# Optimization experiments

Measured on AMD Instinct MI355X. Metric: run time of the kernel, lower is better.

## Reference

```python
import jax, jax.numpy as jnp
import numpy as np

N_NODES = 50000
N_EDGES = 600000
EMB_DIM = 128
HIDDEN = 128
BN_EPS = 1e-5


def setup_inputs() -> dict:
    key = jax.random.key(0)
    ks = jax.random.split(key, 8)
    s_in = 1.0 / np.sqrt(EMB_DIM)
    s_h = 1.0 / np.sqrt(HIDDEN)
    return {
        "x_idx": jnp.arange(N_NODES, dtype=jnp.int32),
        "edge_index": jax.random.randint(ks[0], (2, N_EDGES), 0, N_NODES, dtype=jnp.int32),
        "emb_table": jax.random.normal(ks[1], (N_NODES, EMB_DIM), jnp.float32),
        # ClusterGCNConv: lin_out (bias=False) and lin_root (bias=False)
        "W_out": jax.random.uniform(ks[2], (HIDDEN, EMB_DIM), jnp.float32, -s_in, s_in),
        "W_root": jax.random.uniform(ks[3], (HIDDEN, EMB_DIM), jnp.float32, -s_in, s_in),
        "bn0_gamma": jnp.ones((HIDDEN,), jnp.float32),
        "bn0_beta": jnp.zeros((HIDDEN,), jnp.float32),
        # SGConv 1 (K=1, add_self_loops=True, Linear with bias)
        "W_sg1": jax.random.uniform(ks[4], (HIDDEN, HIDDEN), jnp.float32, -s_h, s_h),
        "b_sg1": jnp.zeros((HIDDEN,), jnp.float32),
        "bn1_gamma": jnp.ones((HIDDEN,), jnp.float32),
        "bn1_beta": jnp.zeros((HIDDEN,), jnp.float32),
        # SGConv 2 (final layer)
        "W_sg2": jax.random.uniform(ks[5], (HIDDEN, HIDDEN), jnp.float32, -s_h, s_h),
        "b_sg2": jnp.zeros((HIDDEN,), jnp.float32),
    }


def _cluster_gcn(x, row, col, W_out, W_root, n):
    # PyG ClusterGCNConv (add_self_loops=False, diag_lambda=0, bias=False):
    # out[c] = sum_{(r->c)} (1/deg(c)) * x[r];  return out @ W_out^T + x @ W_root^T
    deg = jax.ops.segment_sum(jnp.ones_like(col, dtype=x.dtype), col, num_segments=n)
    deg_inv = 1.0 / jnp.maximum(deg, 1.0)
    msg = x[row] * deg_inv[col][:, None]                  # [E, D]
    agg = jax.ops.segment_sum(msg, col, num_segments=n)   # [N, D]
    return agg @ W_out.T + x @ W_root.T


def _sg_conv(x, row, col, W, b, n):
    # PyG SGConv K=1 with gcn_norm: A_hat = D^{-1/2}(A+I)D^{-1/2}, then Linear.
    loop = jnp.arange(n, dtype=row.dtype)
    r = jnp.concatenate([row, loop])
    c = jnp.concatenate([col, loop])
    deg = jax.ops.segment_sum(jnp.ones_like(c, dtype=x.dtype), c, num_segments=n)
    dis = jnp.where(deg > 0, jax.lax.rsqrt(jnp.maximum(deg, 1e-12)), 0.0)
    ew = dis[r] * dis[c]                                   # [E+N]
    agg = jax.ops.segment_sum(x[r] * ew[:, None], c, num_segments=n)
    return agg @ W.T + b


def _bn(x, gamma, beta):
    # BatchNorm1d in training mode: batch statistics, biased variance.
    mu = x.mean(axis=0)
    var = ((x - mu) ** 2).mean(axis=0)
    return (x - mu) * jax.lax.rsqrt(var + BN_EPS) * gamma + beta


def reference(x_idx, edge_index, emb_table, W_out, W_root, bn0_gamma, bn0_beta,
              W_sg1, b_sg1, bn1_gamma, bn1_beta, W_sg2, b_sg2):
    n = emb_table.shape[0]
    row, col = edge_index[0], edge_index[1]
    x = emb_table[x_idx]                                   # [N, D]
    # layer 0: ClusterGCNConv -> BN -> ReLU (dropout p=0)
    x = _cluster_gcn(x, row, col, W_out, W_root, n)
    x = jax.nn.relu(_bn(x, bn0_gamma, bn0_beta))
    # layer 1: SGConv -> BN -> ReLU
    x = _sg_conv(x, row, col, W_sg1, b_sg1, n)
    x = jax.nn.relu(_bn(x, bn1_gamma, bn1_beta))
    # final SGConv
    return _sg_conv(x, row, col, W_sg2, b_sg2, n)
```

## Files before the change

kernel.cpp:

```cpp
#include <hip/hip_runtime.h>
#include <stdint.h>

#define NN 50000
#define NE 600000
#define DD 128
#define BN_EPS 1e-5f

typedef __attribute__((ext_vector_type(8))) short short8;
typedef __attribute__((ext_vector_type(4))) float f32x4;

__device__ __forceinline__ float bf2f(uint16_t u) {
    union { uint32_t u; float f; } v; v.u = ((uint32_t)u) << 16; return v.f;
}
__device__ __forceinline__ uint16_t f2bf(float f) {
    union { float f; uint32_t u; } v; v.f = f;
    return (uint16_t)((v.u + 0x7FFFu + ((v.u >> 16) & 1u)) >> 16);
}
__device__ __forceinline__ float lo16(uint32_t v) { return bf2f((uint16_t)(v & 0xFFFFu)); }
__device__ __forceinline__ float hi16(uint32_t v) { return bf2f((uint16_t)(v >> 16)); }

__global__ void k_zero(uint4* __restrict__ p, int n16) {
    int i = blockIdx.x * 256 + threadIdx.x;
    if (i < n16) p[i] = make_uint4(0u, 0u, 0u, 0u);
}

#define EB ((NE + 255) / 256)
#define VB ((NN * 32) / 256)
#define WB 32
__global__ void k_pre(const int* __restrict__ ei, int* __restrict__ cnt,
                      const int* __restrict__ x_idx, const float* __restrict__ emb,
                      uint16_t* __restrict__ xb,
                      const float* __restrict__ Wa, const float* __restrict__ Wb_,
                      const float* __restrict__ Wc, const float* __restrict__ Wd,
                      uint16_t* __restrict__ wb) {
    int b = blockIdx.x;
    if (b < EB) {
        int e = b * 256 + threadIdx.x;
        if (e < NE) atomicAdd(&cnt[ei[NE + e]], 1);
    } else if (b < EB + VB) {
        int idx = (b - EB) * 256 + threadIdx.x;
        int node = idx >> 5, c4 = (idx & 31) << 2;
        int src = x_idx[node];
        float4 v = *(const float4*)(emb + (size_t)src * DD + c4);
        ushort4 o;
        o.x = f2bf(v.x); o.y = f2bf(v.y); o.z = f2bf(v.z); o.w = f2bf(v.w);
        *(ushort4*)(xb + (size_t)node * DD + c4) = o;
    } else {
        int idx = (b - EB - VB) * 256 + threadIdx.x;
        int w = idx >> 11, rem = idx & 2047;
        const float* src = (w == 0) ? Wa : (w == 1) ? Wb_ : (w == 2) ? Wc : Wd;
        float4 v0 = *(const float4*)(src + rem * 8);
        float4 v1 = *(const float4*)(src + rem * 8 + 4);
        uint4 pk;
        pk.x = (uint32_t)f2bf(v0.x) | ((uint32_t)f2bf(v0.y) << 16);
        pk.y = (uint32_t)f2bf(v0.z) | ((uint32_t)f2bf(v0.w) << 16);
        pk.z = (uint32_t)f2bf(v1.x) | ((uint32_t)f2bf(v1.y) << 16);
        pk.w = (uint32_t)f2bf(v1.z) | ((uint32_t)f2bf(v1.w) << 16);
        *(uint4*)(wb + (size_t)w * 16384 + rem * 8) = pk;
    }
}

__global__ void k_alloc(const int* __restrict__ cnt, int* __restrict__ cursor,
                        int* __restrict__ off, int* __restrict__ fillp,
                        float* __restrict__ deginv, float* __restrict__ dis) {
    int i = blockIdx.x * 256 + threadIdx.x;
    int lane = threadIdx.x & 63;
    int deg = (i < NN) ? cnt[i] : 0;
    int v = deg;
    #pragma unroll
    for (int d = 1; d < 64; d <<= 1) {
        int t = __shfl_up(v, d, 64);
        if (lane >= d) v += t;
    }
    int total = __shfl(v, 63, 64);
    int wbase = 0;
    if (lane == 63) wbase = atomicAdd(cursor, total);
    wbase = __shfl(wbase, 63, 64);
    int base = wbase + v - deg;
    if (i < NN) {
        off[i] = base;
        fillp[i] = base;
        deginv[i] = 1.0f / fmaxf((float)deg, 1.0f);
        dis[i] = rsqrtf((float)deg + 1.0f);
    }
}

__global__ void k_fill(const int* __restrict__ ei, int* __restrict__ fillp,
                       int* __restrict__ csr_row) {
    int e = blockIdx.x * 256 + threadIdx.x;
    if (e < NE) {
        int c = ei[NE + e];
        int p = atomicAdd(&fillp[c], 1);
        csr_row[p] = ei[e];
    }
}

template<int MODE>
__global__ __launch_bounds__(256)
void k_agg(const uint16_t* __restrict__ X, const int* __restrict__ off,
           const int* __restrict__ cnt, const int* __restrict__ csr_row,
           const float* __restrict__ deginv, const float* __restrict__ dis,
           uint16_t* __restrict__ aggb) {
    int gw = blockIdx.x * 4 + (threadIdx.x >> 6);
    int lane = threadIdx.x & 63;
    int hl = lane & 31;
    int node = gw * 2 + (lane >> 5);
    if (node >= NN) return;
    float a0 = 0.0f, a1 = 0.0f, a2 = 0.0f, a3 = 0.0f;
    if (MODE == 1) {
        uint2 v = ((const uint2*)(X + (size_t)node * DD))[hl];
        a0 = lo16(v.x); a1 = hi16(v.x); a2 = lo16(v.y); a3 = hi16(v.y);
    }
    int s = off[node], deg = cnt[node];
    int degO = __shfl(deg, lane ^ 32, 64);
    int mdeg = max(deg, degO);
    for (int b = 0; b < mdeg; b += 32) {
        int c32 = min(deg - b, 32);
        int idxv = (hl < c32) ? csr_row[s + b + hl] : 0;
        int steps = min(mdeg - b, 32);
        int i = 0;
        for (; i + 8 <= steps; i += 8) {
            uint2 v[8]; float w[8];
            #pragma unroll
            for (int u = 0; u < 8; ++u) {
                int r = __shfl(idxv, (lane & 32) + i + u, 64);
                w[u] = (b + i + u < deg) ? 1.0f : 0.0f;
                v[u] = ((const uint2*)(X + (size_t)r * DD))[hl];
            }
            #pragma unroll
            for (int u = 0; u < 8; ++u) {
                a0 = fmaf(w[u], lo16(v[u].x), a0);
                a1 = fmaf(w[u], hi16(v[u].x), a1);
                a2 = fmaf(w[u], lo16(v[u].y), a2);
                a3 = fmaf(w[u], hi16(v[u].y), a3);
            }
        }
        if (i + 4 <= steps) {
            uint2 v[4]; float w[4];
            #pragma unroll
            for (int u = 0; u < 4; ++u) {
                int r = __shfl(idxv, (lane & 32) + i + u, 64);
                w[u] = (b + i + u < deg) ? 1.0f : 0.0f;
                v[u] = ((const uint2*)(X + (size_t)r * DD))[hl];
            }
            #pragma unroll
            for (int u = 0; u < 4; ++u) {
                a0 = fmaf(w[u], lo16(v[u].x), a0);
                a1 = fmaf(w[u], hi16(v[u].x), a1);
                a2 = fmaf(w[u], lo16(v[u].y), a2);
                a3 = fmaf(w[u], hi16(v[u].y), a3);
            }
            i += 4;
        }
        for (; i < steps; ++i) {
            int r = __shfl(idxv, (lane & 32) + i, 64);
            float w = (b + i < deg) ? 1.0f : 0.0f;
            uint2 v = ((const uint2*)(X + (size_t)r * DD))[hl];
            a0 = fmaf(w, lo16(v.x), a0);
            a1 = fmaf(w, hi16(v.x), a1);
            a2 = fmaf(w, lo16(v.y), a2);
            a3 = fmaf(w, hi16(v.y), a3);
        }
    }
    float sc = (MODE == 1) ? dis[node] : deginv[node];
    a0 *= sc; a1 *= sc; a2 *= sc; a3 *= sc;
    uint2 o;
    o.x = (uint32_t)f2bf(a0) | ((uint32_t)f2bf(a1) << 16);
    o.y = (uint32_t)f2bf(a2) | ((uint32_t)f2bf(a3) << 16);
    ((uint2*)(aggb + (size_t)node * DD))[hl] = o;
}

template<bool DUAL, bool STATS, bool BIAS, bool STORE_BF16>
__global__ __launch_bounds__(256, 2)
void k_gemm(const uint16_t* __restrict__ A1, const uint16_t* __restrict__ A2,
            const uint16_t* __restrict__ Wb1, const uint16_t* __restrict__ Wb2,
            const float* __restrict__ bias, float* __restrict__ Hf,
            uint16_t* __restrict__ Hb, float* __restrict__ stats) {
    constexpr int NW = DUAL ? 2 : 1;
    __shared__ uint16_t Wlds[NW * 128 * 128];
    const int t = threadIdx.x;
    const int lane = t & 63, wid = t >> 6;
    const int l15 = lane & 15, kgrp = lane >> 4;
    const int wm = (wid >> 1) * 64, wn = (wid & 1) * 64;
    const int m0 = blockIdx.x * 128;

    short8 a1r[4][4];
    #pragma unroll
    for (int m = 0; m < 4; ++m) {
        int row = min(m0 + wm + m * 16 + l15, NN - 1);
        const uint16_t* ap = A1 + (size_t)row * DD + kgrp * 8;
        #pragma unroll
        for (int ks = 0; ks < 4; ++ks)
            a1r[m][ks] = *(const short8*)(ap + ks * 32);
    }
    #pragma unroll
    for (int w = 0; w < NW; ++w) {
        const uint16_t* Ws = w ? Wb2 : Wb1;
        #pragma unroll
        for (int it = 0; it < 8; ++it) {
            int idx = it * 256 + t;
            int row = idx >> 4, c16 = idx & 15;
            uint4 v = *(const uint4*)(Ws + row * DD + c16 * 8);
            uint32_t boff = (uint32_t)(w * 32768 + row * 256 + ((c16 * 16) ^ ((row & 7) << 4)));
            *(uint4*)((char*)Wlds + boff) = v;
        }
    }
    __syncthreads();

    f32x4 acc[4][4];
    #pragma unroll
    for (int m = 0; m < 4; ++m)
        #pragma unroll
        for (int n = 0; n < 4; ++n) acc[m][n] = f32x4{0.0f, 0.0f, 0.0f, 0.0f};

    short8 a2r[4][4];
    if (DUAL) {
        #pragma unroll
        for (int m = 0; m < 4; ++m) {
            int row = min(m0 + wm + m * 16 + l15, NN - 1);
            const uint16_t* ap = A2 + (size_t)row * DD + kgrp * 8;
            #pragma unroll
            for (int ks = 0; ks < 4; ++ks)
                a2r[m][ks] = *(const short8*)(ap + ks * 32);
        }
    }
    #pragma unroll
    for (int ph = 0; ph < NW; ++ph) {
        #pragma unroll
        for (int ks = 0; ks < 4; ++ks) {
            short8 b[4];
            int kb = ks * 64 + (kgrp << 4);
            #pragma unroll
            for (int n = 0; n < 4; ++n) {
                int row = wn + n * 16 + l15;
                b[n] = *(const short8*)((const char*)Wlds + ph * 32768
                                        + row * 256 + (kb ^ ((row & 7) << 4)));
            }
            #pragma unroll
            for (int m = 0; m < 4; ++m)
                #pragma unroll
                for (int n = 0; n < 4; ++n)
                    acc[m][n] = __builtin_amdgcn_mfma_f32_16x16x32_bf16(
                        (ph ? a2r : a1r)[m][ks], b[n], acc[m][n], 0, 0, 0);
        }
    }
    float* stc = STATS ? stats + (wid & 3) * 256 : nullptr;
    #pragma unroll
    for (int n = 0; n < 4; ++n) {
        int col = wn + n * 16 + l15;
        float bb = BIAS ? bias[col] : 0.0f;
        float ssum = 0.0f, ssq = 0.0f;
        #pragma unroll
        for (int m = 0; m < 4; ++m) {
            int rbase = m0 + wm + m * 16 + kgrp * 4;
            #pragma unroll
            for (int i = 0; i < 4; ++i) {
                int gr = rbase + i;
                if (gr < NN) {
                    float v = acc[m][n][i] + bb;
                    if (STORE_BF16) Hb[(size_t)gr * DD + col] = f2bf(v);
                    else            Hf[(size_t)gr * DD + col] = v;
                    ssum += v; ssq += v * v;
                }
            }
        }
        if (STATS) {
            ssum += __shfl_xor(ssum, 16, 64);
            ssum += __shfl_xor(ssum, 32, 64);
            ssq  += __shfl_xor(ssq, 16, 64);
            ssq  += __shfl_xor(ssq, 32, 64);
            if (lane < 16) {
                atomicAdd(&stc[col], ssum);
                atomicAdd(&stc[128 + col], ssq);
            }
        }
    }
}

__global__ __launch_bounds__(256)
void k_bnrelu(const uint16_t* __restrict__ Hb, const float* __restrict__ st,
              const float* __restrict__ gamma, const float* __restrict__ beta,
              const float* __restrict__ dis, uint16_t* __restrict__ xb) {
    __shared__ float s_sc[128], s_of[128];
    int t = threadIdx.x;
    if (t < 128) {
        const float invn = 1.0f / (float)NN;
        float sum = st[t] + st[256 + t] + st[512 + t] + st[768 + t];
        float sq  = st[128 + t] + st[384 + t] + st[640 + t] + st[896 + t];
        float mean = sum * invn;
        float var = sq * invn - mean * mean;
        float sc = gamma[t] * rsqrtf(var + BN_EPS);
        s_sc[t] = sc;
        s_of[t] = beta[t] - mean * sc;
    }
    __syncthreads();
    int idx = blockIdx.x * 256 + t;
    int node = idx >> 4, c8 = (idx & 15) << 3;
    if (node >= NN) return;
    float d = dis[node];
    uint4 h = *(const uint4*)(Hb + (size_t)node * DD + c8);
    uint32_t hw[4] = {h.x, h.y, h.z, h.w};
    uint32_t ow[4];
    #pragma unroll
    for (int j = 0; j < 4; ++j) {
        int c = c8 + j * 2;
        float v0 = fmaxf(lo16(hw[j]) * s_sc[c]     + s_of[c],     0.0f) * d;
        float v1 = fmaxf(hi16(hw[j]) * s_sc[c + 1] + s_of[c + 1], 0.0f) * d;
        ow[j] = (uint32_t)f2bf(v0) | ((uint32_t)f2bf(v1) << 16);
    }
    uint4 o = make_uint4(ow[0], ow[1], ow[2], ow[3]);
    *(uint4*)(xb + (size_t)node * DD + c8) = o;
}

extern "C" void kernel_launch(void* const* d_in, const int* in_sizes, int n_in,
                              void* d_out, int out_size, void* d_ws, size_t ws_size,
                              hipStream_t stream) {
    const int* x_idx   = (const int*)d_in[0];
    const int* ei      = (const int*)d_in[1];
    const float* emb   = (const float*)d_in[2];
    const float* W_out = (const float*)d_in[3];
    const float* W_root= (const float*)d_in[4];
    const float* g0    = (const float*)d_in[5];
    const float* be0   = (const float*)d_in[6];
    const float* W1    = (const float*)d_in[7];
    const float* b1    = (const float*)d_in[8];
    const float* g1    = (const float*)d_in[9];
    const float* be1   = (const float*)d_in[10];
    const float* W2    = (const float*)d_in[11];
    const float* b2    = (const float*)d_in[12];
    float* out = (float*)d_out;

    char* ws = (char*)d_ws;
    size_t o = 0;
    auto carve = [&](size_t bytes) -> void* {
        void* p = ws + o;
        o = (o + bytes + 255) & ~(size_t)255;
        return p;
    };
    int* cnt      = (int*)carve((size_t)NN * 4);
    int* cursor   = (int*)carve(4);
    float* st0    = (float*)carve(1024 * 4);
    float* st1    = (float*)carve(1024 * 4);
    size_t zlen = o;
    int* fillp    = (int*)carve((size_t)NN * 4);
    int* off      = (int*)carve((size_t)NN * 4);
    float* deginv = (float*)carve((size_t)NN * 4);
    float* dis    = (float*)carve((size_t)NN * 4);
    int* csr_row  = (int*)carve((size_t)NE * 4);
    uint16_t* xb  = (uint16_t*)carve((size_t)NN * DD * 2);
    uint16_t* aggb= (uint16_t*)carve((size_t)NN * DD * 2);
    uint16_t* hb  = (uint16_t*)carve((size_t)NN * DD * 2);
    uint16_t* wb  = (uint16_t*)carve((size_t)4 * 16384 * 2);

    const int ZB = (int)((zlen / 16 + 255) / 256);
    const int NB = (NN + 255) / 256;
    const int GB = (NN + 127) / 128;
    const int AB = (NN / 2 + 3) / 4;
    const int BB = (NN * 16 + 255) / 256;

    k_zero<<<ZB, 256, 0, stream>>>((uint4*)ws, (int)(zlen / 16));
    k_pre<<<EB + VB + WB, 256, 0, stream>>>(ei, cnt, x_idx, emb, xb,
                                            W_out, W_root, W1, W2, wb);
    k_alloc<<<NB, 256, 0, stream>>>(cnt, cursor, off, fillp, deginv, dis);
    k_fill<<<EB, 256, 0, stream>>>(ei, fillp, csr_row);

    k_agg<0><<<AB, 256, 0, stream>>>(xb, off, cnt, csr_row, deginv, dis, aggb);
    k_gemm<true, true, false, true><<<GB, 256, 0, stream>>>(
        aggb, xb, wb, wb + 16384, nullptr, nullptr, hb, st0);
    k_bnrelu<<<BB, 256, 0, stream>>>(hb, st0, g0, be0, dis, xb);

    k_agg<1><<<AB, 256, 0, stream>>>(xb, off, cnt, csr_row, deginv, dis, aggb);
    k_gemm<false, true, true, true><<<GB, 256, 0, stream>>>(
        aggb, nullptr, wb + 32768, nullptr, b1, nullptr, hb, st1);
    k_bnrelu<<<BB, 256, 0, stream>>>(hb, st1, g1, be1, dis, xb);

    k_agg<1><<<AB, 256, 0, stream>>>(xb, off, cnt, csr_row, deginv, dis, aggb);
    k_gemm<false, false, true, false><<<GB, 256, 0, stream>>>(
        aggb, nullptr, wb + 49152, nullptr, b2, out, nullptr, nullptr);
}
```

Measured before the change: 229.2 us.

## Shrink GEMM block tile to 64 rows with 16-row per-wave strips

```diff
diff --git a/kernel.cpp b/kernel.cpp
--- a/kernel.cpp
+++ b/kernel.cpp
@@ -171,7 +171,7 @@
 }
 
 template<bool DUAL, bool STATS, bool BIAS, bool STORE_BF16>
-__global__ __launch_bounds__(256, 2)
+__global__ __launch_bounds__(256, DUAL ? 2 : 4)
 void k_gemm(const uint16_t* __restrict__ A1, const uint16_t* __restrict__ A2,
             const uint16_t* __restrict__ Wb1, const uint16_t* __restrict__ Wb2,
             const float* __restrict__ bias, float* __restrict__ Hf,
@@ -181,17 +181,15 @@
     const int t = threadIdx.x;
     const int lane = t & 63, wid = t >> 6;
     const int l15 = lane & 15, kgrp = lane >> 4;
-    const int wm = (wid >> 1) * 64, wn = (wid & 1) * 64;
-    const int m0 = blockIdx.x * 128;
-
-    short8 a1r[4][4];
-    #pragma unroll
-    for (int m = 0; m < 4; ++m) {
-        int row = min(m0 + wm + m * 16 + l15, NN - 1);
+    const int r0 = blockIdx.x * 64 + wid * 16;
+
+    short8 a1r[4], a2r[4];
+    {
+        int row = min(r0 + l15, NN - 1);
         const uint16_t* ap = A1 + (size_t)row * DD + kgrp * 8;
         #pragma unroll
         for (int ks = 0; ks < 4; ++ks)
-            a1r[m][ks] = *(const short8*)(ap + ks * 32);
+            a1r[ks] = *(const short8*)(ap + ks * 32);
     }
     #pragma unroll
     for (int w = 0; w < NW; ++w) {
@@ -207,61 +205,51 @@
     }
     __syncthreads();
 
-    f32x4 acc[4][4];
-    #pragma unroll
-    for (int m = 0; m < 4; ++m)
-        #pragma unroll
-        for (int n = 0; n < 4; ++n) acc[m][n] = f32x4{0.0f, 0.0f, 0.0f, 0.0f};
-
-    short8 a2r[4][4];
     if (DUAL) {
-        #pragma unroll
-        for (int m = 0; m < 4; ++m) {
-            int row = min(m0 + wm + m * 16 + l15, NN - 1);
-            const uint16_t* ap = A2 + (size_t)row * DD + kgrp * 8;
-            #pragma unroll
-            for (int ks = 0; ks < 4; ++ks)
-                a2r[m][ks] = *(const short8*)(ap + ks * 32);
-        }
-    }
+        int row = min(r0 + l15, NN - 1);
+        const uint16_t* ap = A2 + (size_t)row * DD + kgrp * 8;
+        #pragma unroll
+        for (int ks = 0; ks < 4; ++ks)
+            a2r[ks] = *(const short8*)(ap + ks * 32);
+    }
+
+    f32x4 acc[8];
+    #pragma unroll
+    for (int n = 0; n < 8; ++n) acc[n] = f32x4{0.0f, 0.0f, 0.0f, 0.0f};
+
     #pragma unroll
     for (int ph = 0; ph < NW; ++ph) {
         #pragma unroll
         for (int ks = 0; ks < 4; ++ks) {
-            short8 b[4];
+            short8 b[8];
             int kb = ks * 64 + (kgrp << 4);
             #pragma unroll
-            for (int n = 0; n < 4; ++n) {
-                int row = wn + n * 16 + l15;
+            for (int n = 0; n < 8; ++n) {
+                int row = n * 16 + l15;
                 b[n] = *(const short8*)((const char*)Wlds + ph * 32768
                                         + row * 256 + (kb ^ ((row & 7) << 4)));
             }
             #pragma unroll
-            for (int m = 0; m < 4; ++m)
-                #pragma unroll
-                for (int n = 0; n < 4; ++n)
-                    acc[m][n] = __builtin_amdgcn_mfma_f32_16x16x32_bf16(
-                        (ph ? a2r : a1r)[m][ks], b[n], acc[m][n], 0, 0, 0);
+            for (int n = 0; n < 8; ++n)
+                acc[n] = __builtin_amdgcn_mfma_f32_16x16x32_bf16(
+                    (ph ? a2r : a1r)[ks], b[n], acc[n], 0, 0, 0);
         }
     }
     float* stc = STATS ? stats + (wid & 3) * 256 : nullptr;
     #pragma unroll
-    for (int n = 0; n < 4; ++n) {
-        int col = wn + n * 16 + l15;
+    for (int n = 0; n < 8; ++n) {
+        int col = n * 16 + l15;
         float bb = BIAS ? bias[col] : 0.0f;
         float ssum = 0.0f, ssq = 0.0f;
-        #pragma unroll
-        for (int m = 0; m < 4; ++m) {
-            int rbase = m0 + wm + m * 16 + kgrp * 4;
-            #pragma unroll
-            for (int i = 0; i < 4; ++i) {
-                int gr = rbase + i;
-                if (gr < NN) {
-                    float v = acc[m][n][i] + bb;
-                    if (STORE_BF16) Hb[(size_t)gr * DD + col] = f2bf(v);
-                    else            Hf[(size_t)gr * DD + col] = v;
-                    ssum += v; ssq += v * v;
-                }
+        int rbase = r0 + kgrp * 4;
+        #pragma unroll
+        for (int i = 0; i < 4; ++i) {
+            int gr = rbase + i;
+            if (gr < NN) {
+                float v = acc[n][i] + bb;
+                if (STORE_BF16) Hb[(size_t)gr * DD + col] = f2bf(v);
+                else            Hf[(size_t)gr * DD + col] = v;
+                ssum += v; ssq += v * v;
             }
         }
         if (STATS) {
@@ -354,7 +342,7 @@
 
     const int ZB = (int)((zlen / 16 + 255) / 256);
     const int NB = (NN + 255) / 256;
-    const int GB = (NN + 127) / 128;
+    const int GB = (NN + 63) / 64;
     const int AB = (NN / 2 + 3) / 4;
     const int BB = (NN * 16 + 255) / 256;
 
```

Measured after the change: 251.5 us. 1.1x slower.

## Pre-swizzle bf16 weights and load them into LDS with direct global-to-LDS loads

Applied to the files above, without the earlier changes.

```diff
diff --git a/kernel.cpp b/kernel.cpp
--- a/kernel.cpp
+++ b/kernel.cpp
@@ -56,7 +56,9 @@
         pk.y = (uint32_t)f2bf(v0.z) | ((uint32_t)f2bf(v0.w) << 16);
         pk.z = (uint32_t)f2bf(v1.x) | ((uint32_t)f2bf(v1.y) << 16);
         pk.w = (uint32_t)f2bf(v1.z) | ((uint32_t)f2bf(v1.w) << 16);
-        *(uint4*)(wb + (size_t)w * 16384 + rem * 8) = pk;
+        int row = rem >> 4, c16 = rem & 15;
+        uint32_t boff = (uint32_t)(row * 256 + ((c16 * 16) ^ ((row & 7) << 4)));
+        *(uint4*)((char*)wb + (size_t)w * 32768 + boff) = pk;
     }
 }
 
@@ -171,7 +173,7 @@
 }
 
 template<bool DUAL, bool STATS, bool BIAS, bool STORE_BF16>
-__global__ __launch_bounds__(256, 2)
+__global__ __launch_bounds__(256, DUAL ? 2 : 3)
 void k_gemm(const uint16_t* __restrict__ A1, const uint16_t* __restrict__ A2,
             const uint16_t* __restrict__ Wb1, const uint16_t* __restrict__ Wb2,
             const float* __restrict__ bias, float* __restrict__ Hf,
@@ -184,6 +186,20 @@
     const int wm = (wid >> 1) * 64, wn = (wid & 1) * 64;
     const int m0 = blockIdx.x * 128;
 
+    #pragma unroll
+    for (int w = 0; w < NW; ++w) {
+        const char* Ws = (const char*)(w ? Wb2 : Wb1);
+        char* ldsb = (char*)Wlds + w * 32768;
+        #pragma unroll
+        for (int it = 0; it < 8; ++it) {
+            int base_chunk = it * 256 + (t & 192);
+            int lane_chunk = base_chunk + (t & 63);
+            __builtin_amdgcn_global_load_lds(
+                (const __attribute__((address_space(1))) uint32_t*)(Ws + (size_t)lane_chunk * 16),
+                (__attribute__((address_space(3))) uint32_t*)(uint32_t)(uintptr_t)(ldsb + base_chunk * 16),
+                16, 0, 0);
+        }
+    }
     short8 a1r[4][4];
     #pragma unroll
     for (int m = 0; m < 4; ++m) {
@@ -192,18 +208,6 @@
         #pragma unroll
         for (int ks = 0; ks < 4; ++ks)
             a1r[m][ks] = *(const short8*)(ap + ks * 32);
-    }
-    #pragma unroll
-    for (int w = 0; w < NW; ++w) {
-        const uint16_t* Ws = w ? Wb2 : Wb1;
-        #pragma unroll
-        for (int it = 0; it < 8; ++it) {
-            int idx = it * 256 + t;
-            int row = idx >> 4, c16 = idx & 15;
-            uint4 v = *(const uint4*)(Ws + row * DD + c16 * 8);
-            uint32_t boff = (uint32_t)(w * 32768 + row * 256 + ((c16 * 16) ^ ((row & 7) << 4)));
-            *(uint4*)((char*)Wlds + boff) = v;
-        }
     }
     __syncthreads();
 
@@ -244,7 +248,7 @@
                         (ph ? a2r : a1r)[m][ks], b[n], acc[m][n], 0, 0, 0);
         }
     }
-    float* stc = STATS ? stats + (wid & 3) * 256 : nullptr;
+    float* stc = STATS ? stats + ((wid + ((blockIdx.x & 1) << 2)) & 7) * 256 : nullptr;
     #pragma unroll
     for (int n = 0; n < 4; ++n) {
         int col = wn + n * 16 + l15;
@@ -285,8 +289,12 @@
     int t = threadIdx.x;
     if (t < 128) {
         const float invn = 1.0f / (float)NN;
-        float sum = st[t] + st[256 + t] + st[512 + t] + st[768 + t];
-        float sq  = st[128 + t] + st[384 + t] + st[640 + t] + st[896 + t];
+        float sum = 0.0f, sq = 0.0f;
+        #pragma unroll
+        for (int k = 0; k < 8; ++k) {
+            sum += st[k * 256 + t];
+            sq  += st[k * 256 + 128 + t];
+        }
         float mean = sum * invn;
         float var = sq * invn - mean * mean;
         float sc = gamma[t] * rsqrtf(var + BN_EPS);
@@ -339,8 +347,8 @@
     };
     int* cnt      = (int*)carve((size_t)NN * 4);
     int* cursor   = (int*)carve(4);
-    float* st0    = (float*)carve(1024 * 4);
-    float* st1    = (float*)carve(1024 * 4);
+    float* st0    = (float*)carve(2048 * 4);
+    float* st1    = (float*)carve(2048 * 4);
     size_t zlen = o;
     int* fillp    = (int*)carve((size_t)NN * 4);
     int* off      = (int*)carve((size_t)NN * 4);
```

After: 222.5 us, median of 2. 2.9% less time.
